# Kernel tuning notes

Measured on AMD Instinct MI355X. Metric: run time of the kernel, lower is better.

Reference implementation:

```python
import jax, jax.numpy as jnp
import numpy as np

ROLE_BITS = 20
NHEAD = 16
D_MODEL = 1024
D_KEY = D_MODEL // NHEAD  # 64
D_FIL = 512
DFF = 4096
EPS = 1e-5


def _ln(x, g, b):
    mu = jnp.mean(x, axis=-1, keepdims=True)
    var = jnp.mean(jnp.square(x - mu), axis=-1, keepdims=True)
    return (x - mu) * jax.lax.rsqrt(var + EPS) * g + b


def setup_inputs() -> dict:
    key = jax.random.key(0)
    ks = jax.random.split(key, 10)
    N, BSZ, MEM = 16384, 16, 8
    D_IN = D_FIL + ROLE_BITS  # 532
    values = jax.random.normal(ks[0], (N, D_FIL), jnp.float32)
    role_index = jax.random.randint(ks[1], (N,), 1, 2 ** ROLE_BITS)
    # every (batch, memory_slot) pair occupied -> static shapes (compression is a no-op)
    slot = jax.random.permutation(ks[2], jnp.tile(jnp.arange(BSZ * MEM), N // (BSZ * MEM)))
    batch_index = (slot // MEM).astype(jnp.int32)
    memory_index = (slot % MEM).astype(jnp.int32)
    query_vectors = jax.random.normal(ks[3], (NHEAD, D_KEY), jnp.float32) * (1.0 / np.sqrt(D_KEY))
    s = 0.02
    Wk = jax.random.normal(ks[4], (D_MODEL, D_IN), jnp.float32) * s
    Wv = jax.random.normal(ks[5], (D_MODEL, D_IN), jnp.float32) * s
    Wo = jax.random.normal(ks[6], (D_MODEL, D_MODEL), jnp.float32) * s
    W1 = jax.random.normal(ks[7], (DFF, D_MODEL), jnp.float32) * s
    W2 = jax.random.normal(ks[8], (D_MODEL, DFF), jnp.float32) * s
    return dict(
        values=values, role_index=role_index, batch_index=batch_index,
        memory_index=memory_index, query_vectors=query_vectors,
        Wk=Wk, Wv=Wv, Wo=Wo, bo=jnp.zeros((D_MODEL,), jnp.float32),
        W1=W1, b1=jnp.zeros((DFF,), jnp.float32),
        W2=W2, b2=jnp.zeros((D_MODEL,), jnp.float32),
        g_fil=jnp.ones((D_FIL,), jnp.float32), b_fil=jnp.zeros((D_FIL,), jnp.float32),
        g_mha=jnp.ones((D_IN,), jnp.float32), b_mha=jnp.zeros((D_IN,), jnp.float32),
        g_ff=jnp.ones((D_MODEL,), jnp.float32), b_ff=jnp.zeros((D_MODEL,), jnp.float32),
        g_out=jnp.ones((D_MODEL,), jnp.float32), b_out=jnp.zeros((D_MODEL,), jnp.float32),
        bsz=BSZ, memory_slots=MEM,
    )


def _tree_positional_encodings(role_index):
    # bit-expand role indices: column j is bit j of the role index
    bits = (jnp.bitwise_and(role_index[:, None], 2 ** jnp.arange(ROLE_BITS)) != 0).astype(jnp.float32)
    # locate the highest set bit (torch: flip + argmax)
    mi = jnp.argmax(bits[:, ::-1], axis=1)
    cm = ROLE_BITS - 1 - mi  # index of highest set bit
    bits = bits * (1.0 - jax.nn.one_hot(cm, ROLE_BITS, dtype=bits.dtype))  # zero it out
    branch = jnp.arange(ROLE_BITS)[None, :] < cm[:, None]
    return jnp.where(branch, (bits - 0.5) * 2.0, bits)  # {0,1} -> {-1,1} below MSB


def reference(values, role_index, batch_index, memory_index, query_vectors,
              Wk, Wv, Wo, bo, W1, b1, W2, b2,
              g_fil, b_fil, g_mha, b_mha, g_ff, b_ff, g_out, b_out,
              bsz, memory_slots):
    N = values.shape[0]
    T = bsz * memory_slots  # num_trees (all (batch, slot) pairs occupied)

    tpd = _tree_positional_encodings(role_index)
    x = jnp.concatenate([_ln(values, g_fil, b_fil), tpd], axis=1)  # [N, d_input]
    x = _ln(x, g_mha, b_mha)
    k = (x @ Wk.T).reshape(N, NHEAD, D_KEY)
    v = (x @ Wv.T).reshape(N, NHEAD, D_KEY)
    qkm = jnp.einsum('nhd,hd->nh', k, query_vectors)  # [N, H]

    # combined batch+memory mask: node n attends to flat tree t = b*mem + m
    node_slot = batch_index * memory_slots + memory_index  # [N]
    mask = node_slot[:, None] == jnp.arange(T)[None, :]  # [N, T]
    scores = jnp.where(mask[:, :, None], qkm[:, None, :], -1e9) / np.sqrt(D_KEY)
    attn = jax.nn.softmax(scores, axis=0)  # softmax over nodes, [N, T, H]
    out = jnp.einsum('nhv,nth->thv', v, attn).reshape(T, D_MODEL)

    # post-attention: proj_o + residual with flattened queries, LN, FF, LN
    r1 = (out @ Wo.T + bo) + query_vectors.reshape(-1)
    l1 = _ln(r1, g_ff, b_ff)
    ff = jax.nn.gelu(l1 @ W1.T + b1, approximate=False) @ W2.T + b2
    l2 = _ln(ff + r1, g_out, b_out)

    rectangle_out = l2.reshape(bsz, memory_slots, D_MODEL)
    agent_pad_mask = jnp.zeros((bsz, memory_slots), dtype=bool)
    return rectangle_out, agent_pad_mask
```

## Files before the change

kernel.cpp:

```cpp
#include <hip/hip_runtime.h>
#include <hip/hip_bf16.h>

typedef __hip_bfloat16 bf16;

#define N_NODES 16384
#define D_FIL 512
#define D_IN 532
#define D_MODEL 1024
#define NHEAD 16
#define D_KEY 64
#define DFF 4096
#define NTREE 128
#define MEM_SLOTS 8
#define NODES_PER_TREE 128
#define EPS 1e-5f
#define XSE 544
#define XSU 272
#define CSTR 32
#define BSTR 40

typedef float f32x4 __attribute__((ext_vector_type(4)));
typedef short s16x8 __attribute__((ext_vector_type(8)));

union PackU { uint4 u; s16x8 s; };

__device__ inline float gelu_exact(float x) {
    return 0.5f * x * (1.0f + erff(x * 0.7071067811865476f));
}

__device__ inline void blockReduceSum2_512(float& a, float& b, float* sm) {
    int tid = threadIdx.x;
    int lane = tid & 63, wid = tid >> 6;
#pragma unroll
    for (int off = 32; off > 0; off >>= 1) {
        a += __shfl_down(a, off, 64);
        b += __shfl_down(b, off, 64);
    }
    if (lane == 0) { sm[wid] = a; sm[8 + wid] = b; }
    __syncthreads();
    if (tid == 0) {
        float s0 = 0.f, s1 = 0.f;
#pragma unroll
        for (int i = 0; i < 8; ++i) { s0 += sm[i]; s1 += sm[8 + i]; }
        sm[16] = s0; sm[17] = s1;
    }
    __syncthreads();
    a = sm[16]; b = sm[17];
}

__global__ __launch_bounds__(256) void prep_kernel(
        const float* __restrict__ values, const int* __restrict__ role,
        const int* __restrict__ bidx, const int* __restrict__ midx,
        const float* __restrict__ g_fil, const float* __restrict__ b_fil,
        const float* __restrict__ g_mha, const float* __restrict__ b_mha,
        bf16* __restrict__ xs, int* __restrict__ counts,
        const float* __restrict__ q, const float* __restrict__ Wk,
        unsigned* __restrict__ wqb,
        const float* __restrict__ Wv, float* __restrict__ wvt) {
    int b = blockIdx.x;
    int tid = threadIdx.x;

    if (b < 16) {
        int h = b;
        __shared__ float qs[64];
        if (tid < 64) qs[tid] = q[h * 64 + tid];
        __syncthreads();
        for (int p = tid; p < XSU; p += 256) {
            unsigned out = 0u;
            if (p < 266) {
                float a0 = 0.f, a1 = 0.f;
                int j0 = 2 * p;
#pragma unroll 8
                for (int d = 0; d < 64; ++d) {
                    const float* wr = Wk + (size_t)(h * 64 + d) * D_IN;
                    a0 += qs[d] * wr[j0];
                    a1 += qs[d] * wr[j0 + 1];
                }
                unsigned u0 = (unsigned)__bfloat16_as_ushort(__float2bfloat16(a0));
                unsigned u1 = (unsigned)__bfloat16_as_ushort(__float2bfloat16(a1));
                out = (u1 << 16) | u0;
            }
            wqb[h * XSU + p] = out;
        }
        return;
    }

    if (b < 560) {
        __shared__ float tile[32][33];
        int vb = b - 16;
        int c0 = (vb & 31) * 32, j0 = (vb >> 5) * 32;
        int tx = tid & 31, ty = tid >> 5;
#pragma unroll
        for (int r = 0; r < 4; ++r) {
            int cc = ty + r * 8;
            int j = j0 + tx;
            tile[cc][tx] = (j < D_IN) ? Wv[(size_t)(c0 + cc) * D_IN + j] : 0.f;
        }
        __syncthreads();
#pragma unroll
        for (int r = 0; r < 4; ++r) {
            int j = j0 + ty + r * 8;
            if (j < D_IN) wvt[(size_t)j * D_MODEL + c0 + tx] = tile[tx][ty + r * 8];
        }
        return;
    }

    int wave = tid >> 6;
    int l = tid & 63;
    int n = (b - 560) * 4 + wave;

    const float4* vp = (const float4*)(values + (size_t)n * D_FIL + l * 8);
    float4 v0 = vp[0], v1 = vp[1];

    int row = 0;
    if (l == 0) {
        int slot = bidx[n] * MEM_SLOTS + midx[n];
        int pos = atomicAdd(&counts[slot * CSTR], 1);
        row = slot * NODES_PER_TREE + pos;
    }

    float s = v0.x + v0.y + v0.z + v0.w + v1.x + v1.y + v1.z + v1.w;
    float ss = v0.x * v0.x + v0.y * v0.y + v0.z * v0.z + v0.w * v0.w
             + v1.x * v1.x + v1.y * v1.y + v1.z * v1.z + v1.w * v1.w;
#pragma unroll
    for (int m = 1; m < 64; m <<= 1) {
        s += __shfl_xor(s, m, 64);
        ss += __shfl_xor(ss, m, 64);
    }
    float mu = s * (1.f / D_FIL);
    float var = ss * (1.f / D_FIL) - mu * mu;
    float rs = rsqrtf(var + EPS);

    const float4* gf = (const float4*)(g_fil + l * 8);
    const float4* bf = (const float4*)(b_fil + l * 8);
    float4 gf0 = gf[0], gf1 = gf[1], bf0 = bf[0], bf1 = bf[1];
    float y[8];
    y[0] = (v0.x - mu) * rs * gf0.x + bf0.x;
    y[1] = (v0.y - mu) * rs * gf0.y + bf0.y;
    y[2] = (v0.z - mu) * rs * gf0.z + bf0.z;
    y[3] = (v0.w - mu) * rs * gf0.w + bf0.w;
    y[4] = (v1.x - mu) * rs * gf1.x + bf1.x;
    y[5] = (v1.y - mu) * rs * gf1.y + bf1.y;
    y[6] = (v1.z - mu) * rs * gf1.z + bf1.z;
    y[7] = (v1.w - mu) * rs * gf1.w + bf1.w;

    int r = role[n];
    int cm = 31 - __clz(r);
    float s_t = 2.f * (float)(__popc(r) - 1) - (float)cm;
    float ss_t = (float)cm;

    float s2 = y[0] + y[1] + y[2] + y[3] + y[4] + y[5] + y[6] + y[7];
    float ss2 = y[0] * y[0] + y[1] * y[1] + y[2] * y[2] + y[3] * y[3]
              + y[4] * y[4] + y[5] * y[5] + y[6] * y[6] + y[7] * y[7];
#pragma unroll
    for (int m = 1; m < 64; m <<= 1) {
        s2 += __shfl_xor(s2, m, 64);
        ss2 += __shfl_xor(ss2, m, 64);
    }
    s2 += s_t; ss2 += ss_t;
    float mu2 = s2 * (1.f / D_IN);
    float var2 = ss2 * (1.f / D_IN) - mu2 * mu2;
    float rs2 = rsqrtf(var2 + EPS);

    const float4* gm = (const float4*)(g_mha + l * 8);
    const float4* bm = (const float4*)(b_mha + l * 8);
    float4 gm0 = gm[0], gm1 = gm[1], bm0 = bm[0], bm1 = bm[1];
    float x[8];
    x[0] = (y[0] - mu2) * rs2 * gm0.x + bm0.x;
    x[1] = (y[1] - mu2) * rs2 * gm0.y + bm0.y;
    x[2] = (y[2] - mu2) * rs2 * gm0.z + bm0.z;
    x[3] = (y[3] - mu2) * rs2 * gm0.w + bm0.w;
    x[4] = (y[4] - mu2) * rs2 * gm1.x + bm1.x;
    x[5] = (y[5] - mu2) * rs2 * gm1.y + bm1.y;
    x[6] = (y[6] - mu2) * rs2 * gm1.z + bm1.z;
    x[7] = (y[7] - mu2) * rs2 * gm1.w + bm1.w;

    row = __shfl(row, 0, 64);

    {
        unsigned us[8];
#pragma unroll
        for (int k = 0; k < 8; ++k)
            us[k] = (unsigned)__bfloat16_as_ushort(__float2bfloat16(x[k]));
        uint4 pk = make_uint4((us[1] << 16) | us[0], (us[3] << 16) | us[2],
                              (us[5] << 16) | us[4], (us[7] << 16) | us[6]);
        *(uint4*)((char*)xs + (size_t)row * (XSE * 2) + 16 * l) = pk;
    }

    if (l < 20) {
        int bit = (r >> l) & 1;
        float tpd = (l < cm) ? (bit ? 1.f : -1.f) : 0.f;
        float x2 = (tpd - mu2) * rs2 * g_mha[512 + l] + b_mha[512 + l];
        xs[(size_t)row * XSE + 512 + l] = __float2bfloat16(x2);
    } else if (l < 26) {
        ((unsigned*)xs)[(size_t)row * XSU + 266 + (l - 20)] = 0u;
    }
}

__global__ __launch_bounds__(256) void attn_fused_kernel(const unsigned* __restrict__ xsu,
                                                         const unsigned* __restrict__ wqb,
                                                         const float* __restrict__ wvt,
                                                         float* __restrict__ attn_out) {
    int f = blockIdx.x;
    int xcd = f & 7;
    int hg = (f >> 3) & 3;
    int t = (f >> 5) * 8 + xcd;
    int tid = threadIdx.x;
    __shared__ __align__(16) float a4[NODES_PER_TREE * 4];
    __shared__ __align__(16) char sbuf[8576];
    unsigned* wsh = (unsigned*)sbuf;
    float (*zs)[536] = (float(*)[536])sbuf;

    for (int i = tid; i < 4 * 274; i += 256) {
        int hh = i / 274, p = i - hh * 274;
        wsh[hh * 274 + p] = (p < XSU) ? wqb[(hg * 4 + hh) * XSU + p] : 0u;
    }
    __syncthreads();

    {
        int i = tid >> 2, hh = tid & 3;
        const uint2* xr0 = (const uint2*)(xsu + (size_t)(t * NODES_PER_TREE + i) * XSU);
        const uint2* xr1 = (const uint2*)(xsu + (size_t)(t * NODES_PER_TREE + i + 64) * XSU);
        const uint2* wr  = (const uint2*)(wsh + hh * 274);
        float a0 = 0.f, a1 = 0.f;
#pragma unroll 8
        for (int j = 0; j < 133; ++j) {
            uint2 wu = wr[j];
            uint2 xa = xr0[j];
            uint2 xb = xr1[j];
            float w0 = __uint_as_float(wu.x << 16), w1 = __uint_as_float(wu.x & 0xffff0000u);
            float w2 = __uint_as_float(wu.y << 16), w3 = __uint_as_float(wu.y & 0xffff0000u);
            a0 += __uint_as_float(xa.x << 16) * w0 + __uint_as_float(xa.x & 0xffff0000u) * w1
                + __uint_as_float(xa.y << 16) * w2 + __uint_as_float(xa.y & 0xffff0000u) * w3;
            a1 += __uint_as_float(xb.x << 16) * w0 + __uint_as_float(xb.x & 0xffff0000u) * w1
                + __uint_as_float(xb.y << 16) * w2 + __uint_as_float(xb.y & 0xffff0000u) * w3;
        }
        a4[tid] = a0 * 0.125f;
        a4[tid + 256] = a1 * 0.125f;
    }
    __syncthreads();

    int hh = tid >> 6, lane = tid & 63;
    {
        float s0 = a4[lane * 4 + hh], s1 = a4[(lane + 64) * 4 + hh];
        float m = fmaxf(s0, s1);
#pragma unroll
        for (int off = 32; off > 0; off >>= 1) m = fmaxf(m, __shfl_xor(m, off, 64));
        float e0 = expf(s0 - m), e1 = expf(s1 - m);
        float sum = e0 + e1;
#pragma unroll
        for (int off = 32; off > 0; off >>= 1) sum += __shfl_xor(sum, off, 64);
        float inv = 1.0f / sum;
        a4[lane * 4 + hh] = e0 * inv;
        a4[(lane + 64) * 4 + hh] = e1 * inv;
    }
    __syncthreads();

    {
        bool hasT = tid < 10;
        float az[4][2] = {};
        float at[4][2] = {};
        const unsigned* xt = xsu + (size_t)t * NODES_PER_TREE * XSU;
        for (int i0 = 0; i0 < NODES_PER_TREE; i0 += 8) {
            unsigned u[8], u2[8];
            float4 av[8];
#pragma unroll
            for (int k = 0; k < 8; ++k) u[k] = xt[(size_t)(i0 + k) * XSU + tid];
#pragma unroll
            for (int k = 0; k < 8; ++k) u2[k] = hasT ? xt[(size_t)(i0 + k) * XSU + 256 + tid] : 0u;
#pragma unroll
            for (int k = 0; k < 8; ++k) av[k] = *(const float4*)(a4 + (i0 + k) * 4);
#pragma unroll
            for (int k = 0; k < 8; ++k) {
                float x0 = __uint_as_float(u[k] << 16);
                float x1 = __uint_as_float(u[k] & 0xffff0000u);
                float x2 = __uint_as_float(u2[k] << 16);
                float x3 = __uint_as_float(u2[k] & 0xffff0000u);
                float4 a = av[k];
                az[0][0] += a.x * x0; az[0][1] += a.x * x1;
                az[1][0] += a.y * x0; az[1][1] += a.y * x1;
                az[2][0] += a.z * x0; az[2][1] += a.z * x1;
                az[3][0] += a.w * x0; az[3][1] += a.w * x1;
                at[0][0] += a.x * x2; at[0][1] += a.x * x3;
                at[1][0] += a.y * x2; at[1][1] += a.y * x3;
                at[2][0] += a.z * x2; at[2][1] += a.z * x3;
                at[3][0] += a.w * x2; at[3][1] += a.w * x3;
            }
        }
        __syncthreads();
#pragma unroll
        for (int k = 0; k < 4; ++k) {
            *(float2*)(&zs[k][2 * tid]) = make_float2(az[k][0], az[k][1]);
            if (hasT) *(float2*)(&zs[k][512 + 2 * tid]) = make_float2(at[k][0], at[k][1]);
        }
    }
    __syncthreads();

    int c = hg * 256 + tid;
    const float* wp = wvt + c;
    float acc0 = 0.f, acc1 = 0.f;
    for (int j0 = 0; j0 < 528; j0 += 8) {
        float wv[8];
#pragma unroll
        for (int k = 0; k < 8; ++k) wv[k] = wp[(size_t)(j0 + k) * D_MODEL];
#pragma unroll
        for (int k = 0; k < 8; k += 2) {
            acc0 += zs[hh][j0 + k] * wv[k];
            acc1 += zs[hh][j0 + k + 1] * wv[k + 1];
        }
    }
    {
        float wv[4];
#pragma unroll
        for (int k = 0; k < 4; ++k) wv[k] = wp[(size_t)(528 + k) * D_MODEL];
#pragma unroll
        for (int k = 0; k < 4; k += 2) {
            acc0 += zs[hh][528 + k] * wv[k];
            acc1 += zs[hh][528 + k + 1] * wv[k + 1];
        }
    }
    attn_out[(size_t)t * D_MODEL + c] = acc0 + acc1;
}

__global__ __launch_bounds__(256) void gemm_mfma_sk(const float* __restrict__ A,
                                                    const float* __restrict__ B,
                                                    float* __restrict__ Cpart,
                                                    int N, int K, int nsb) {
    __shared__ __align__(16) unsigned short bhi[32 * BSTR];
    __shared__ __align__(16) unsigned short blo[32 * BSTR];
    int tid = threadIdx.x;
    int col0 = blockIdx.x * 32;
    int k0 = blockIdx.y * nsb * 32;
    float* C = Cpart + (size_t)blockIdx.y * 128 * N;

    int w = tid >> 6, l = tid & 63;
    int l15 = l & 15, l4 = l >> 4;
    int scol = tid >> 3, sk4 = (tid & 7) * 4;

    f32x4 acc[2][2];
#pragma unroll
    for (int rt = 0; rt < 2; ++rt)
#pragma unroll
        for (int ct = 0; ct < 2; ++ct) acc[rt][ct] = (f32x4){0.f, 0.f, 0.f, 0.f};

    for (int s = 0; s < nsb; ++s) {
        int kb = k0 + s * 32;

        const float* bp = B + (size_t)(col0 + scol) * K + kb + sk4;
        float4 fb = *(const float4*)bp;

        float4 fa[2][2];
#pragma unroll
        for (int rt = 0; rt < 2; ++rt) {
            const float* ap = A + (size_t)(32 * w + 16 * rt + l15) * K + kb + l4 * 8;
            fa[rt][0] = *(const float4*)ap;
            fa[rt][1] = *(const float4*)(ap + 4);
        }

        {
            float fe[4] = {fb.x, fb.y, fb.z, fb.w};
            unsigned hu[2], lu[2];
#pragma unroll
            for (int p = 0; p < 2; ++p) {
                unsigned u0 = __float_as_uint(fe[2 * p]);
                unsigned u1 = __float_as_uint(fe[2 * p + 1]);
                unsigned h0 = u0 & 0xffff0000u, h1 = u1 & 0xffff0000u;
                float d0 = fe[2 * p] - __uint_as_float(h0);
                float d1 = fe[2 * p + 1] - __uint_as_float(h1);
                hu[p] = h1 | (u0 >> 16);
                lu[p] = (__float_as_uint(d1) & 0xffff0000u) | (__float_as_uint(d0) >> 16);
            }
            *(uint2*)(&bhi[scol * BSTR + sk4]) = make_uint2(hu[0], hu[1]);
            *(uint2*)(&blo[scol * BSTR + sk4]) = make_uint2(lu[0], lu[1]);
        }
        __syncthreads();

        s16x8 ah[2], al[2];
#pragma unroll
        for (int rt = 0; rt < 2; ++rt) {
            float fe[8] = {fa[rt][0].x, fa[rt][0].y, fa[rt][0].z, fa[rt][0].w,
                           fa[rt][1].x, fa[rt][1].y, fa[rt][1].z, fa[rt][1].w};
            unsigned hu[4], lu[4];
#pragma unroll
            for (int p = 0; p < 4; ++p) {
                unsigned u0 = __float_as_uint(fe[2 * p]);
                unsigned u1 = __float_as_uint(fe[2 * p + 1]);
                unsigned h0 = u0 & 0xffff0000u, h1 = u1 & 0xffff0000u;
                float d0 = fe[2 * p] - __uint_as_float(h0);
                float d1 = fe[2 * p + 1] - __uint_as_float(h1);
                hu[p] = h1 | (u0 >> 16);
                lu[p] = (__float_as_uint(d1) & 0xffff0000u) | (__float_as_uint(d0) >> 16);
            }
            PackU uh, ul;
            uh.u = make_uint4(hu[0], hu[1], hu[2], hu[3]);
            ul.u = make_uint4(lu[0], lu[1], lu[2], lu[3]);
            ah[rt] = uh.s;
            al[rt] = ul.s;
        }

#pragma unroll
        for (int ct = 0; ct < 2; ++ct) {
            PackU rbh, rbl;
            rbh.u = *(const uint4*)(&bhi[(16 * ct + l15) * BSTR + l4 * 8]);
            rbl.u = *(const uint4*)(&blo[(16 * ct + l15) * BSTR + l4 * 8]);
#pragma unroll
            for (int rt = 0; rt < 2; ++rt) {
                acc[rt][ct] = __builtin_amdgcn_mfma_f32_16x16x32_bf16(ah[rt], rbh.s, acc[rt][ct], 0, 0, 0);
                acc[rt][ct] = __builtin_amdgcn_mfma_f32_16x16x32_bf16(al[rt], rbh.s, acc[rt][ct], 0, 0, 0);
                acc[rt][ct] = __builtin_amdgcn_mfma_f32_16x16x32_bf16(ah[rt], rbl.s, acc[rt][ct], 0, 0, 0);
            }
        }
        __syncthreads();
    }

#pragma unroll
    for (int rt = 0; rt < 2; ++rt) {
        int row = 32 * w + 16 * rt + l4 * 4;
#pragma unroll
        for (int ct = 0; ct < 2; ++ct) {
            int col = col0 + 16 * ct + l15;
#pragma unroll
            for (int r = 0; r < 4; ++r)
                C[(size_t)(row + r) * N + col] = acc[rt][ct][r];
        }
    }
}

__global__ __launch_bounds__(512) void ln_r1_kernel(const float* __restrict__ po, const float* __restrict__ bo,
                             const float* __restrict__ qvec, const float* __restrict__ g,
                             const float* __restrict__ b, float* __restrict__ r1,
                             float* __restrict__ l1) {
    int t = blockIdx.x, tid = threadIdx.x;
    __shared__ float sm[18];
    float e[2];
#pragma unroll
    for (int c = 0; c < 2; ++c) {
        int j = c * 512 + tid;
        float v = bo[j] + qvec[j];
#pragma unroll
        for (int s = 0; s < 8; ++s)
            v += po[(size_t)s * NTREE * D_MODEL + (size_t)t * D_MODEL + j];
        e[c] = v;
        r1[(size_t)t * D_MODEL + j] = v;
    }
    float s = e[0] + e[1];
    float ss = e[0] * e[0] + e[1] * e[1];
    blockReduceSum2_512(s, ss, sm);
    float mu = s * (1.f / D_MODEL);
    float var = ss * (1.f / D_MODEL) - mu * mu;
    float rs = rsqrtf(var + EPS);
#pragma unroll
    for (int c = 0; c < 2; ++c) {
        int j = c * 512 + tid;
        l1[(size_t)t * D_MODEL + j] = (e[c] - mu) * rs * g[j] + b[j];
    }
}

__global__ void gelu_reduce_kernel(const float* __restrict__ p1, const float* __restrict__ b1,
                                   float* __restrict__ h1) {
    int idx4 = (blockIdx.x * 256 + threadIdx.x) * 4;
    int col = idx4 & (DFF - 1);
    float4 v = *(const float4*)(b1 + col);
#pragma unroll
    for (int s = 0; s < 4; ++s) {
        float4 p = *(const float4*)(p1 + (size_t)s * NTREE * DFF + idx4);
        v.x += p.x; v.y += p.y; v.z += p.z; v.w += p.w;
    }
    v.x = gelu_exact(v.x); v.y = gelu_exact(v.y);
    v.z = gelu_exact(v.z); v.w = gelu_exact(v.w);
    *(float4*)(h1 + idx4) = v;
}

__global__ __launch_bounds__(512) void ln_out_kernel(const float* __restrict__ p2, const float* __restrict__ b2,
                              const float* __restrict__ r1, const float* __restrict__ g,
                              const float* __restrict__ b, float* __restrict__ out) {
    int t = blockIdx.x, tid = threadIdx.x;
    __shared__ float sm[18];
    float e[2];
#pragma unroll
    for (int c = 0; c < 2; ++c) {
        int j = c * 512 + tid;
        float v = b2[j] + r1[(size_t)t * D_MODEL + j];
#pragma unroll
        for (int s = 0; s < 16; ++s)
            v += p2[(size_t)s * NTREE * D_MODEL + (size_t)t * D_MODEL + j];
        e[c] = v;
    }
    float s = e[0] + e[1];
    float ss = e[0] * e[0] + e[1] * e[1];
    blockReduceSum2_512(s, ss, sm);
    float mu = s * (1.f / D_MODEL);
    float var = ss * (1.f / D_MODEL) - mu * mu;
    float rs = rsqrtf(var + EPS);
#pragma unroll
    for (int c = 0; c < 2; ++c) {
        int j = c * 512 + tid;
        out[(size_t)t * D_MODEL + j] = (e[c] - mu) * rs * g[j] + b[j];
    }
    if (t == 0 && tid < 128) out[(size_t)NTREE * D_MODEL + tid] = 0.f;
}

extern "C" void kernel_launch(void* const* d_in, const int* in_sizes, int n_in,
                              void* d_out, int out_size, void* d_ws, size_t ws_size,
                              hipStream_t stream) {
    const float* values = (const float*)d_in[0];
    const int* role     = (const int*)d_in[1];
    const int* bidx     = (const int*)d_in[2];
    const int* midx     = (const int*)d_in[3];
    const float* qvec   = (const float*)d_in[4];
    const float* Wk     = (const float*)d_in[5];
    const float* Wv     = (const float*)d_in[6];
    const float* Wo     = (const float*)d_in[7];
    const float* bo     = (const float*)d_in[8];
    const float* W1     = (const float*)d_in[9];
    const float* b1     = (const float*)d_in[10];
    const float* W2     = (const float*)d_in[11];
    const float* b2     = (const float*)d_in[12];
    const float* g_fil  = (const float*)d_in[13];
    const float* b_fil  = (const float*)d_in[14];
    const float* g_mha  = (const float*)d_in[15];
    const float* b_mha  = (const float*)d_in[16];
    const float* g_ff   = (const float*)d_in[17];
    const float* b_ff   = (const float*)d_in[18];
    const float* g_out  = (const float*)d_in[19];
    const float* b_out  = (const float*)d_in[20];

    char* w = (char*)d_ws;
    int*   counts   = (int*)(w + 0);
    unsigned* wqb   = (unsigned*)(w + 16384);
    float* attn_out = (float*)(w + 34816);
    float* r1       = (float*)(w + 559104);
    float* l1       = (float*)(w + 1083392);
    float* h1       = (float*)(w + 1607680);
    float* wvt      = (float*)(w + 3704832);
    char*  big      = w + 5883904;
    bf16*  xs = (bf16*)big;
    float* po = (float*)big;
    float* p1 = (float*)(big + 4194304);
    float* p2 = (float*)big;

    float* out = (float*)d_out;

    hipMemsetAsync(counts, 0, 16384, stream);

    prep_kernel<<<4656, 256, 0, stream>>>(values, role, bidx, midx,
                                          g_fil, b_fil, g_mha, b_mha,
                                          xs, counts,
                                          qvec, Wk, wqb, Wv, wvt);

    attn_fused_kernel<<<512, 256, 0, stream>>>((const unsigned*)xs, wqb, wvt, attn_out);

    gemm_mfma_sk<<<dim3(32, 8), 256, 0, stream>>>(attn_out, Wo, po, D_MODEL, D_MODEL, 4);

    ln_r1_kernel<<<NTREE, 512, 0, stream>>>(po, bo, qvec, g_ff, b_ff, r1, l1);

    gemm_mfma_sk<<<dim3(128, 4), 256, 0, stream>>>(l1, W1, p1, DFF, D_MODEL, 8);

    gelu_reduce_kernel<<<512, 256, 0, stream>>>(p1, b1, h1);

    gemm_mfma_sk<<<dim3(32, 16), 256, 0, stream>>>(h1, W2, p2, D_MODEL, DFF, 8);

    ln_out_kernel<<<NTREE, 512, 0, stream>>>(p2, b2, r1, g_out, b_out, out);
}
```

Before: 231.4 us.

## Split attention kernel into 2-head groups across twice as many blocks

```diff
diff --git a/kernel.cpp b/kernel.cpp
--- a/kernel.cpp
+++ b/kernel.cpp
@@ -203,46 +203,41 @@
                                                          float* __restrict__ attn_out) {
     int f = blockIdx.x;
     int xcd = f & 7;
-    int hg = (f >> 3) & 3;
-    int t = (f >> 5) * 8 + xcd;
+    int hg2 = (f >> 3) & 7;
+    int t = (f >> 6) * 8 + xcd;
     int tid = threadIdx.x;
-    __shared__ __align__(16) float a4[NODES_PER_TREE * 4];
-    __shared__ __align__(16) char sbuf[8576];
+    __shared__ __align__(16) float a2[256];
+    __shared__ __align__(16) char sbuf[4352];
     unsigned* wsh = (unsigned*)sbuf;
     float (*zs)[536] = (float(*)[536])sbuf;
 
-    for (int i = tid; i < 4 * 274; i += 256) {
+    for (int i = tid; i < 2 * 274; i += 256) {
         int hh = i / 274, p = i - hh * 274;
-        wsh[hh * 274 + p] = (p < XSU) ? wqb[(hg * 4 + hh) * XSU + p] : 0u;
+        wsh[hh * 274 + p] = (p < XSU) ? wqb[(hg2 * 2 + hh) * XSU + p] : 0u;
     }
     __syncthreads();
 
     {
-        int i = tid >> 2, hh = tid & 3;
-        const uint2* xr0 = (const uint2*)(xsu + (size_t)(t * NODES_PER_TREE + i) * XSU);
-        const uint2* xr1 = (const uint2*)(xsu + (size_t)(t * NODES_PER_TREE + i + 64) * XSU);
-        const uint2* wr  = (const uint2*)(wsh + hh * 274);
-        float a0 = 0.f, a1 = 0.f;
+        int i = tid >> 1, hh = tid & 1;
+        const uint2* xr = (const uint2*)(xsu + (size_t)(t * NODES_PER_TREE + i) * XSU);
+        const uint2* wr = (const uint2*)(wsh + hh * 274);
+        float a0 = 0.f;
 #pragma unroll 8
         for (int j = 0; j < 133; ++j) {
             uint2 wu = wr[j];
-            uint2 xa = xr0[j];
-            uint2 xb = xr1[j];
+            uint2 xa = xr[j];
             float w0 = __uint_as_float(wu.x << 16), w1 = __uint_as_float(wu.x & 0xffff0000u);
             float w2 = __uint_as_float(wu.y << 16), w3 = __uint_as_float(wu.y & 0xffff0000u);
             a0 += __uint_as_float(xa.x << 16) * w0 + __uint_as_float(xa.x & 0xffff0000u) * w1
                 + __uint_as_float(xa.y << 16) * w2 + __uint_as_float(xa.y & 0xffff0000u) * w3;
-            a1 += __uint_as_float(xb.x << 16) * w0 + __uint_as_float(xb.x & 0xffff0000u) * w1
-                + __uint_as_float(xb.y << 16) * w2 + __uint_as_float(xb.y & 0xffff0000u) * w3;
-        }
-        a4[tid] = a0 * 0.125f;
-        a4[tid + 256] = a1 * 0.125f;
-    }
-    __syncthreads();
-
-    int hh = tid >> 6, lane = tid & 63;
-    {
-        float s0 = a4[lane * 4 + hh], s1 = a4[(lane + 64) * 4 + hh];
+        }
+        a2[tid] = a0 * 0.125f;
+    }
+    __syncthreads();
+
+    if (tid < 128) {
+        int hh = tid >> 6, lane = tid & 63;
+        float s0 = a2[lane * 2 + hh], s1 = a2[(lane + 64) * 2 + hh];
         float m = fmaxf(s0, s1);
 #pragma unroll
         for (int off = 32; off > 0; off >>= 1) m = fmaxf(m, __shfl_xor(m, off, 64));
@@ -251,75 +246,72 @@
 #pragma unroll
         for (int off = 32; off > 0; off >>= 1) sum += __shfl_xor(sum, off, 64);
         float inv = 1.0f / sum;
-        a4[lane * 4 + hh] = e0 * inv;
-        a4[(lane + 64) * 4 + hh] = e1 * inv;
+        a2[lane * 2 + hh] = e0 * inv;
+        a2[(lane + 64) * 2 + hh] = e1 * inv;
     }
     __syncthreads();
 
     {
         bool hasT = tid < 10;
-        float az[4][2] = {};
-        float at[4][2] = {};
+        float az[2][2] = {};
+        float at[2][2] = {};
         const unsigned* xt = xsu + (size_t)t * NODES_PER_TREE * XSU;
         for (int i0 = 0; i0 < NODES_PER_TREE; i0 += 8) {
             unsigned u[8], u2[8];
-            float4 av[8];
+            float2 av[8];
 #pragma unroll
             for (int k = 0; k < 8; ++k) u[k] = xt[(size_t)(i0 + k) * XSU + tid];
 #pragma unroll
             for (int k = 0; k < 8; ++k) u2[k] = hasT ? xt[(size_t)(i0 + k) * XSU + 256 + tid] : 0u;
 #pragma unroll
-            for (int k = 0; k < 8; ++k) av[k] = *(const float4*)(a4 + (i0 + k) * 4);
+            for (int k = 0; k < 8; ++k) av[k] = *(const float2*)(a2 + (i0 + k) * 2);
 #pragma unroll
             for (int k = 0; k < 8; ++k) {
                 float x0 = __uint_as_float(u[k] << 16);
                 float x1 = __uint_as_float(u[k] & 0xffff0000u);
                 float x2 = __uint_as_float(u2[k] << 16);
                 float x3 = __uint_as_float(u2[k] & 0xffff0000u);
-                float4 a = av[k];
+                float2 a = av[k];
                 az[0][0] += a.x * x0; az[0][1] += a.x * x1;
                 az[1][0] += a.y * x0; az[1][1] += a.y * x1;
-                az[2][0] += a.z * x0; az[2][1] += a.z * x1;
-                az[3][0] += a.w * x0; az[3][1] += a.w * x1;
                 at[0][0] += a.x * x2; at[0][1] += a.x * x3;
                 at[1][0] += a.y * x2; at[1][1] += a.y * x3;
-                at[2][0] += a.z * x2; at[2][1] += a.z * x3;
-                at[3][0] += a.w * x2; at[3][1] += a.w * x3;
             }
         }
         __syncthreads();
 #pragma unroll
-        for (int k = 0; k < 4; ++k) {
+        for (int k = 0; k < 2; ++k) {
             *(float2*)(&zs[k][2 * tid]) = make_float2(az[k][0], az[k][1]);
             if (hasT) *(float2*)(&zs[k][512 + 2 * tid]) = make_float2(at[k][0], at[k][1]);
         }
     }
     __syncthreads();
 
-    int c = hg * 256 + tid;
-    const float* wp = wvt + c;
-    float acc0 = 0.f, acc1 = 0.f;
-    for (int j0 = 0; j0 < 528; j0 += 8) {
-        float wv[8];
-#pragma unroll
-        for (int k = 0; k < 8; ++k) wv[k] = wp[(size_t)(j0 + k) * D_MODEL];
-#pragma unroll
-        for (int k = 0; k < 8; k += 2) {
-            acc0 += zs[hh][j0 + k] * wv[k];
-            acc1 += zs[hh][j0 + k + 1] * wv[k + 1];
-        }
-    }
     {
-        float wv[4];
-#pragma unroll
-        for (int k = 0; k < 4; ++k) wv[k] = wp[(size_t)(528 + k) * D_MODEL];
-#pragma unroll
-        for (int k = 0; k < 4; k += 2) {
-            acc0 += zs[hh][528 + k] * wv[k];
-            acc1 += zs[hh][528 + k + 1] * wv[k + 1];
-        }
-    }
-    attn_out[(size_t)t * D_MODEL + c] = acc0 + acc1;
+        int cc = tid & 127, jh = tid >> 7;
+        int lh = cc >> 6;
+        const float* wp = wvt + hg2 * 128 + cc;
+        const float* zp = &zs[lh][0];
+        int jbeg = jh ? 268 : 0;
+        int jend = jh ? 532 : 268;
+        float acc0 = 0.f, acc1 = 0.f;
+        int j0 = jbeg;
+        for (; j0 + 8 <= jend; j0 += 8) {
+            float wv[8];
+#pragma unroll
+            for (int k = 0; k < 8; ++k) wv[k] = wp[(size_t)(j0 + k) * D_MODEL];
+#pragma unroll
+            for (int k = 0; k < 8; k += 2) {
+                acc0 += zp[j0 + k] * wv[k];
+                acc1 += zp[j0 + k + 1] * wv[k + 1];
+            }
+        }
+        for (; j0 < jend; ++j0) acc0 += zp[j0] * wp[(size_t)j0 * D_MODEL];
+        a2[tid] = acc0 + acc1;
+    }
+    __syncthreads();
+    if (tid < 128)
+        attn_out[(size_t)t * D_MODEL + hg2 * 128 + tid] = a2[tid] + a2[tid + 128];
 }
 
 __global__ __launch_bounds__(256) void gemm_mfma_sk(const float* __restrict__ A,
@@ -548,7 +540,7 @@
                                           xs, counts,
                                           qvec, Wk, wqb, Wv, wvt);
 
-    attn_fused_kernel<<<512, 256, 0, stream>>>((const unsigned*)xs, wqb, wvt, attn_out);
+    attn_fused_kernel<<<1024, 256, 0, stream>>>((const unsigned*)xs, wqb, wvt, attn_out);
 
     gemm_mfma_sk<<<dim3(32, 8), 256, 0, stream>>>(attn_out, Wo, po, D_MODEL, D_MODEL, 4);
 
```

Measured after the change: 237.7 us. 2.7% more time.
